# Optimization experiments

Hardware: AMD Instinct MI355X
Metric: run time of the kernel (lower is better)

Reference implementation:

```python
import jax, jax.numpy as jnp
import numpy as np

D_MODEL, D_INNER, D_STATE, D_CONV, DT_RANK = 1024, 2048, 16, 4, 64
BATCH, SEQLEN = 4, 2048


def setup_inputs() -> dict:
    key = jax.random.key(0)
    ks = jax.random.split(key, 10)
    def n(k, shape, scale=1.0):
        return (jax.random.normal(k, shape, dtype=jnp.float32) * scale)
    # A_log = log of positive values in (0, d_state] like the torch init
    A_log = jnp.log(jax.random.uniform(ks[7], (D_INNER, D_STATE), dtype=jnp.float32, minval=0.5, maxval=float(D_STATE)))
    return {
        "hidden_states": n(ks[0], (BATCH, SEQLEN, D_MODEL)),
        "in_proj_w": n(ks[1], (2 * D_INNER, D_MODEL), D_MODEL ** -0.5),
        "conv_w": n(ks[2], (D_INNER, D_CONV), D_CONV ** -0.5),
        "conv_b": n(ks[3], (D_INNER,), 0.1),
        "x_proj_w": n(ks[4], (DT_RANK + 2 * D_STATE, D_INNER), D_INNER ** -0.5),
        "dt_proj_w": n(ks[5], (D_INNER, DT_RANK), DT_RANK ** -0.5),
        "dt_proj_b": n(ks[6], (D_INNER,), 0.5),
        "A_log": A_log,
        "D": jnp.ones((D_INNER,), dtype=jnp.float32),
        "out_proj_w": n(ks[8], (D_MODEL, D_INNER), D_INNER ** -0.5),
    }


def _silu(x):
    return x * jax.nn.sigmoid(x)


def _mamba_forward(hidden_states, in_proj_w, conv_w, conv_b, x_proj_w,
                   dt_proj_w, dt_proj_b, A_log, D, out_proj_w):
    B, L, _ = hidden_states.shape
    d_inner, d_conv = conv_w.shape
    d_state = A_log.shape[1]
    dt_rank = dt_proj_w.shape[1]

    # in_proj (no bias): (b, l, 2*d_inner)
    xz = jnp.einsum('bld,ed->ble', hidden_states, in_proj_w)
    x, z = xz[..., :d_inner], xz[..., d_inner:]

    # causal depthwise conv1d (padding = d_conv-1, truncated to L) + SiLU
    x_pad = jnp.pad(x, ((0, 0), (d_conv - 1, 0), (0, 0)))  # (b, L+d_conv-1, d)
    x_conv = sum(x_pad[:, w:w + L, :] * conv_w[:, w] for w in range(d_conv)) + conv_b
    x_conv = _silu(x_conv)  # (b, l, d_inner)

    # x_proj -> dt, B, C
    x_dbl = jnp.einsum('bld,ed->ble', x_conv, x_proj_w)  # (b, l, dt_rank+2*d_state)
    dt_in = x_dbl[..., :dt_rank]
    Bv = x_dbl[..., dt_rank:dt_rank + d_state]  # (b, l, n)
    Cv = x_dbl[..., dt_rank + d_state:]         # (b, l, n)

    delta = jax.nn.softplus(jnp.einsum('blr,dr->bld', dt_in, dt_proj_w) + dt_proj_b)
    A = -jnp.exp(A_log)  # (d, n), entries negative

    # selective scan over time: state h is (b, d, n)
    def step(h, inp):
        d_t, B_t, C_t, u_t = inp  # (b,d), (b,n), (b,n), (b,d)
        dA = jnp.exp(d_t[:, :, None] * A)                          # (b, d, n)
        h = h * dA + (d_t * u_t)[:, :, None] * B_t[:, None, :]     # (b, d, n)
        y = jnp.einsum('bdn,bn->bd', h, C_t)                       # (b, d)
        return h, y

    h0 = jnp.zeros((B, d_inner, d_state), dtype=hidden_states.dtype)
    xs = (jnp.swapaxes(delta, 0, 1), jnp.swapaxes(Bv, 0, 1),
          jnp.swapaxes(Cv, 0, 1), jnp.swapaxes(x_conv, 0, 1))
    _, ys = jax.lax.scan(step, h0, xs)  # (l, b, d)
    y = jnp.swapaxes(ys, 0, 1) + x_conv * D  # skip term D * u
    y = y * _silu(z)                           # gating

    # out_proj (no bias)
    return jnp.einsum('bld,md->blm', y, out_proj_w)


def reference(hidden_states, in_proj_w, conv_w, conv_b, x_proj_w,
              dt_proj_w, dt_proj_b, A_log, D, out_proj_w):
    return _mamba_forward(hidden_states, in_proj_w, conv_w, conv_b, x_proj_w,
                          dt_proj_w, dt_proj_b, A_log, D, out_proj_w)
```

## Files before the change

kernel.cpp:

```cpp
#include <hip/hip_runtime.h>
#include <hip/hip_bf16.h>

constexpr int BATCH = 4, SEQLEN = 2048, DM = 1024, DI = 2048, DS = 16, DC = 4, DTR = 64;
constexpr int M = BATCH * SEQLEN;
constexpr int NXZ = 2 * DI;
constexpr int NXDBL = DTR + 2 * DS;
constexpr int CL = 64;
constexpr int NCH = SEQLEN / CL;
constexpr size_t CS = (size_t)BATCH * DI * DS;
constexpr float L2E = 1.44269504088896f;

typedef __attribute__((ext_vector_type(8))) short short8;
typedef __attribute__((ext_vector_type(4))) float f32x4;
typedef __attribute__((ext_vector_type(2))) float f32x2;

__device__ __forceinline__ float fexp2(float x) { return __builtin_amdgcn_exp2f(x); }
__device__ __forceinline__ float frcp(float x) { return __builtin_amdgcn_rcpf(x); }
__device__ __forceinline__ float fsig(float z) {
  return frcp(1.f + fexp2(-L2E * z));
}
__device__ __forceinline__ float softplus_fast(float x) {
  return (x > 20.f) ? x
                    : 0.693147180559945f * __builtin_amdgcn_logf(1.f + fexp2(x * L2E));
}

__device__ __forceinline__ void load_lds16(const void* g, void* l) {
  __builtin_amdgcn_global_load_lds(
      (const __attribute__((address_space(1))) unsigned int*)g,
      (__attribute__((address_space(3))) unsigned int*)l, 16, 0, 0);
}

__global__ __launch_bounds__(256) void k_cvt(const float* __restrict__ s,
                                             __hip_bfloat16* __restrict__ d, int n) {
  int i = (blockIdx.x * 256 + threadIdx.x) * 8;
  if (i + 7 < n) {
    float4 v0 = *reinterpret_cast<const float4*>(s + i);
    float4 v1 = *reinterpret_cast<const float4*>(s + i + 4);
    unsigned short o[8];
    o[0] = __bfloat16_as_ushort(__float2bfloat16(v0.x));
    o[1] = __bfloat16_as_ushort(__float2bfloat16(v0.y));
    o[2] = __bfloat16_as_ushort(__float2bfloat16(v0.z));
    o[3] = __bfloat16_as_ushort(__float2bfloat16(v0.w));
    o[4] = __bfloat16_as_ushort(__float2bfloat16(v1.x));
    o[5] = __bfloat16_as_ushort(__float2bfloat16(v1.y));
    o[6] = __bfloat16_as_ushort(__float2bfloat16(v1.z));
    o[7] = __bfloat16_as_ushort(__float2bfloat16(v1.w));
    *reinterpret_cast<short8*>(d + i) = *reinterpret_cast<short8*>(o);
  }
}

__global__ __launch_bounds__(256) void k_cvt4(const float* __restrict__ p0, int n0, __hip_bfloat16* __restrict__ q0,
                                              const float* __restrict__ p1, int n1, __hip_bfloat16* __restrict__ q1,
                                              const float* __restrict__ p2, int n2, __hip_bfloat16* __restrict__ q2,
                                              const float* __restrict__ p3, int n3, __hip_bfloat16* __restrict__ q3) {
  int i = (blockIdx.x * 256 + threadIdx.x) * 8;
  const float* s;
  __hip_bfloat16* d;
  if (i < n0) { s = p0; d = q0; }
  else if ((i -= n0) < n1) { s = p1; d = q1; }
  else if ((i -= n1) < n2) { s = p2; d = q2; }
  else if ((i -= n2) < n3) { s = p3; d = q3; }
  else return;
  float4 v0 = *reinterpret_cast<const float4*>(s + i);
  float4 v1 = *reinterpret_cast<const float4*>(s + i + 4);
  unsigned short o[8];
  o[0] = __bfloat16_as_ushort(__float2bfloat16(v0.x));
  o[1] = __bfloat16_as_ushort(__float2bfloat16(v0.y));
  o[2] = __bfloat16_as_ushort(__float2bfloat16(v0.z));
  o[3] = __bfloat16_as_ushort(__float2bfloat16(v0.w));
  o[4] = __bfloat16_as_ushort(__float2bfloat16(v1.x));
  o[5] = __bfloat16_as_ushort(__float2bfloat16(v1.y));
  o[6] = __bfloat16_as_ushort(__float2bfloat16(v1.z));
  o[7] = __bfloat16_as_ushort(__float2bfloat16(v1.w));
  *reinterpret_cast<short8*>(d + i) = *reinterpret_cast<short8*>(o);
}

__global__ __launch_bounds__(256) void k_prep(const float* __restrict__ alog,
                                              float* __restrict__ an,
                                              const float* __restrict__ cw,
                                              float* __restrict__ cwt) {
  int i = blockIdx.x * 256 + threadIdx.x;
  if (i < DI * DS) {
    an[i] = -__expf(alog[i]) * L2E;
  } else {
    int j = i - DI * DS;
    if (j < DI * DC) {
      int d = j >> 2, w = j & 3;
      cwt[w * DI + d] = cw[j];
    }
  }
}

template <int BN, int OUTMODE, bool SWZ>
__global__ __launch_bounds__(512, 2) void k_gemmp(const __hip_bfloat16* __restrict__ A, int lda,
                                                  const __hip_bfloat16* __restrict__ Bm, int ldb,
                                                  void* __restrict__ Cp, int ldc, int K) {
  constexpr int BK = 64;
  constexpr int ASLOT = 16384;
  constexpr int BSLOT = BN * BK;
  constexpr int FN = (BN / 4) / 16;
  constexpr int BBASE = 2 * ASLOT;

  const int tid = threadIdx.x;
  const int wid = tid >> 6, l = tid & 63;
  const int wr = wid >> 2, wc = wid & 3;

  int bx = blockIdx.x, by = blockIdx.y;
  if constexpr (SWZ) {
    const int gx = gridDim.x;
    int nlin = by * gx + bx;
    const int nwg = gx * gridDim.y;
    nlin = (nlin & 7) * (nwg >> 3) + (nlin >> 3);
    by = nlin / gx; bx = nlin % gx;
  }
  const int bm0 = by * 256, bn0 = bx * BN;
  const int NT = K / BK;

  __shared__ short LDS[2 * (ASLOT + BSLOT)];

  const int gc8 = (l & 7) ^ ((l >> 3) & 7);
  const __hip_bfloat16* Abase = A + (size_t)(bm0 + wid * 8 + (l >> 3)) * lda + gc8 * 8;
  const __hip_bfloat16* Bbase = Bm + (size_t)(bn0 + wid * 8 + (l >> 3)) * ldb + gc8 * 8;
  const int wslot = wid * 512;

  const int c8k0 = ((l >> 4) ^ (l & 7)) * 8;
  const int c8k1 = ((4 + (l >> 4)) ^ (l & 7)) * 8;
  const int aoff0 = wr * 8192 + (l & 15) * 64;
  const int boff0 = BBASE + wc * (BN / 4) * 64 + (l & 15) * 64;

  f32x4 acc[8][FN] = {};

  auto stageA = [&](int s, int kt) {
#pragma unroll
    for (int g = 0; g < 4; g++)
      load_lds16(Abase + (size_t)(g * 64) * lda + kt * BK,
                 &LDS[s * ASLOT + g * 4096 + wslot]);
  };
  auto stageB = [&](int s, int kt) {
#pragma unroll
    for (int g = 0; g < BN / 64; g++)
      load_lds16(Bbase + (size_t)(g * 64) * ldb + kt * BK,
                 &LDS[BBASE + s * BSLOT + g * 4096 + wslot]);
  };

  stageA(0, 0); stageB(0, 0);

  for (int t = 0; t < NT; t++) {
    const int d = t & 1;
    asm volatile("s_waitcnt vmcnt(0)" ::: "memory");
    __builtin_amdgcn_s_barrier();
    if (t + 1 < NT) { stageA(d ^ 1, t + 1); stageB(d ^ 1, t + 1); }

    const int adb = d * ASLOT + aoff0;
    const int bdb = d * BSLOT + boff0;
    short8 a0[4][2], a1[4][2], b[FN][2];
#pragma unroll
    for (int i = 0; i < 4; i++) {
      a0[i][0] = *reinterpret_cast<const short8*>(&LDS[adb + i * 1024 + c8k0]);
      a0[i][1] = *reinterpret_cast<const short8*>(&LDS[adb + i * 1024 + c8k1]);
    }
#pragma unroll
    for (int j = 0; j < FN; j++) {
      b[j][0] = *reinterpret_cast<const short8*>(&LDS[bdb + j * 1024 + c8k0]);
      b[j][1] = *reinterpret_cast<const short8*>(&LDS[bdb + j * 1024 + c8k1]);
    }
#pragma unroll
    for (int i = 0; i < 4; i++) {
      a1[i][0] = *reinterpret_cast<const short8*>(&LDS[adb + (4 + i) * 1024 + c8k0]);
      a1[i][1] = *reinterpret_cast<const short8*>(&LDS[adb + (4 + i) * 1024 + c8k1]);
    }
#pragma unroll
    for (int i = 0; i < 4; i++)
#pragma unroll
      for (int j = 0; j < FN; j++)
#pragma unroll
        for (int ks = 0; ks < 2; ks++) {
          acc[i][j] = __builtin_amdgcn_mfma_f32_16x16x32_bf16(a0[i][ks], b[j][ks], acc[i][j], 0, 0, 0);
          acc[4 + i][j] = __builtin_amdgcn_mfma_f32_16x16x32_bf16(a1[i][ks], b[j][ks], acc[4 + i][j], 0, 0, 0);
        }
  }

  const int crow0 = bm0 + wr * 128 + (l >> 4) * 4;
  const int ccol0 = bn0 + wc * (BN / 4) + (l & 15);
#pragma unroll
  for (int im = 0; im < 8; im++)
#pragma unroll
    for (int jn = 0; jn < FN; jn++) {
      const int col = ccol0 + jn * 16;
#pragma unroll
      for (int r = 0; r < 4; r++) {
        const int row = crow0 + im * 16 + r;
        float v = acc[im][jn][r];
        if constexpr (OUTMODE == 0)
          reinterpret_cast<float*>(Cp)[(size_t)row * ldc + col] = v;
        else
          reinterpret_cast<__hip_bfloat16*>(Cp)[(size_t)row * ldc + col] = __float2bfloat16(v);
      }
    }
}

template <int BM, int BN, int OUTMODE>
__global__ __launch_bounds__(256) void k_gemm_dl(const __hip_bfloat16* __restrict__ A, int lda,
                                                 const __hip_bfloat16* __restrict__ Bm, int ldb,
                                                 void* __restrict__ Cp, int ldc, int K,
                                                 const float* __restrict__ bias) {
  constexpr int BK = 32;
  constexpr int WM = BM / 2, WN = BN / 2;
  constexpr int FM = WM / 16, FN = WN / 16;

  const int tid = threadIdx.x;
  const int wid = tid >> 6, lane = tid & 63;
  const int wm = wid >> 1, wn = wid & 1;
  const int bm0 = blockIdx.y * BM, bn0 = blockIdx.x * BN;
  int kz = 0;
  if constexpr (OUTMODE == 4) kz = blockIdx.z;

  __shared__ short As[BM * BK];
  __shared__ short Bs[BN * BK];

  f32x4 acc[FM][FN] = {};

  const int lrow = lane & 15;
  const int lk = (lane >> 4) * 8;
  const int srow = wid * 16 + (lane >> 2);
  const int scol = (lane & 3) * 8;

  const __hip_bfloat16* Ag = &A[(size_t)(bm0 + srow) * lda + scol + (size_t)kz * K];
  const __hip_bfloat16* Bg = &Bm[(size_t)(bn0 + srow) * ldb + scol + (size_t)kz * K];

  for (int k0 = 0; k0 < K; k0 += BK) {
    __syncthreads();
#pragma unroll
    for (int i = 0; i < (BM + 63) / 64; i++)
      load_lds16(Ag + (size_t)i * 64 * lda + k0, &As[(i * 64 + wid * 16) * BK]);
#pragma unroll
    for (int i = 0; i < (BN + 63) / 64; i++)
      if ((BN % 64 == 0) || (i * 64 + wid * 16 < BN))
        load_lds16(Bg + (size_t)i * 64 * ldb + k0, &Bs[(i * 64 + wid * 16) * BK]);
    __syncthreads();

    short8 af[FM], bf[FN];
#pragma unroll
    for (int i = 0; i < FM; i++)
      af[i] = *reinterpret_cast<const short8*>(&As[(wm * WM + i * 16 + lrow) * BK + lk]);
#pragma unroll
    for (int j = 0; j < FN; j++)
      bf[j] = *reinterpret_cast<const short8*>(&Bs[(wn * WN + j * 16 + lrow) * BK + lk]);
#pragma unroll
    for (int i = 0; i < FM; i++)
#pragma unroll
      for (int j = 0; j < FN; j++)
        acc[i][j] = __builtin_amdgcn_mfma_f32_16x16x32_bf16(af[i], bf[j], acc[i][j], 0, 0, 0);
  }

  const int crow0 = bm0 + wm * WM + (lane >> 4) * 4;
  const int ccol0 = bn0 + wn * WN + lrow;
#pragma unroll
  for (int i = 0; i < FM; i++)
#pragma unroll
    for (int j = 0; j < FN; j++) {
      const int col = ccol0 + j * 16;
      float bv = 0.f;
      if constexpr (OUTMODE == 2) bv = bias[col];
#pragma unroll
      for (int r = 0; r < 4; r++) {
        const int row = crow0 + i * 16 + r;
        float v = acc[i][j][r];
        if constexpr (OUTMODE == 0) {
          reinterpret_cast<float*>(Cp)[(size_t)row * ldc + col] = v;
        } else if constexpr (OUTMODE == 2) {
          reinterpret_cast<__hip_bfloat16*>(Cp)[(size_t)row * ldc + col] =
              __float2bfloat16(softplus_fast(v + bv));
        } else {
          reinterpret_cast<float*>(Cp)[(size_t)kz * M * NXDBL + (size_t)row * ldc + col] = v;
        }
      }
    }
}

__global__ __launch_bounds__(256) void k_xred(const float* __restrict__ part,
                                              float* __restrict__ xdbl,
                                              __hip_bfloat16* __restrict__ dtin) {
  int i = (blockIdx.x * 256 + threadIdx.x) * 4;
  float4 s = *reinterpret_cast<const float4*>(part + i);
#pragma unroll
  for (int p = 1; p < 8; p++) {
    const float4 v = *reinterpret_cast<const float4*>(part + (size_t)p * M * NXDBL + i);
    s.x += v.x; s.y += v.y; s.z += v.z; s.w += v.w;
  }
  *reinterpret_cast<float4*>(xdbl + i) = s;
  int c = i % NXDBL;
  if (c < DTR) {
    int m = i / NXDBL;
    __hip_bfloat16* dp = dtin + (size_t)m * DTR + c;
    dp[0] = __float2bfloat16(s.x);
    dp[1] = __float2bfloat16(s.y);
    dp[2] = __float2bfloat16(s.z);
    dp[3] = __float2bfloat16(s.w);
  }
}

__global__ __launch_bounds__(256) void k_conv8(const __hip_bfloat16* __restrict__ xz,
                                               const float* __restrict__ cwt,
                                               const float* __restrict__ cb,
                                               __hip_bfloat16* __restrict__ xc) {
  const int ml = blockIdx.x;
  const int d0 = threadIdx.x * 8;
  const int l = ml & (SEQLEN - 1);
  float acc[8];
  {
    float4 b0 = *reinterpret_cast<const float4*>(cb + d0);
    float4 b1 = *reinterpret_cast<const float4*>(cb + d0 + 4);
    acc[0] = b0.x; acc[1] = b0.y; acc[2] = b0.z; acc[3] = b0.w;
    acc[4] = b1.x; acc[5] = b1.y; acc[6] = b1.z; acc[7] = b1.w;
  }
#pragma unroll
  for (int w = 0; w < DC; w++) {
    int li = l - 3 + w;
    if (li >= 0) {
      short8 xv = *reinterpret_cast<const short8*>(&xz[(size_t)(ml - 3 + w) * NXZ + d0]);
      float4 w0 = *reinterpret_cast<const float4*>(cwt + w * DI + d0);
      float4 w1 = *reinterpret_cast<const float4*>(cwt + w * DI + d0 + 4);
      float wf[8] = {w0.x, w0.y, w0.z, w0.w, w1.x, w1.y, w1.z, w1.w};
#pragma unroll
      for (int j = 0; j < 8; j++) {
        float x = __bfloat162float(__ushort_as_bfloat16((unsigned short)xv[j]));
        acc[j] = fmaf(x, wf[j], acc[j]);
      }
    }
  }
  unsigned short o[8];
#pragma unroll
  for (int j = 0; j < 8; j++)
    o[j] = __bfloat16_as_ushort(__float2bfloat16(acc[j] * fsig(acc[j])));
  *reinterpret_cast<short8*>(&xc[(size_t)ml * DI + d0]) = *reinterpret_cast<short8*>(o);
}

__global__ __launch_bounds__(256) void k_scan1(const __hip_bfloat16* __restrict__ delta_b,
                                               const float* __restrict__ xdbl,
                                               const __hip_bfloat16* __restrict__ xc,
                                               const float* __restrict__ Aneg2,
                                               __hip_bfloat16* __restrict__ Pb,
                                               __hip_bfloat16* __restrict__ Sb) {
  const int tid = threadIdx.x;
  const int d = blockIdx.x * 256 + tid;
  const int c = blockIdx.y, b = blockIdx.z;
  const size_t row0 = (size_t)b * SEQLEN + (size_t)c * CL;

  __shared__ float Bs[CL][16];
  {
    int i = tid * 4;
    int li = i >> 4, n0 = i & 15;
    const float* src = &xdbl[(row0 + li) * NXDBL + DTR + n0];
    *reinterpret_cast<float4*>(&Bs[li][n0]) = *reinterpret_cast<const float4*>(src);
  }

  f32x2 Ar2[8];
#pragma unroll
  for (int p = 0; p < 8; p++)
    Ar2[p] = *reinterpret_cast<const f32x2*>(&Aneg2[d * DS + 2 * p]);
  __syncthreads();

  f32x2 h2[8] = {};
  float sdelta = 0.f;
  size_t idx = row0 * DI + d;
  float nx_dt = __bfloat162float(delta_b[idx]);
  float nx_u = __bfloat162float(xc[idx]);
  for (int ls = 0; ls < CL; ls++) {
    float delta = nx_dt;
    float u = nx_u;
    if (ls + 1 < CL) {
      size_t idx2 = idx + DI;
      nx_dt = __bfloat162float(delta_b[idx2]);
      nx_u = __bfloat162float(xc[idx2]);
    }
    idx += DI;
    sdelta += delta;
    float du = delta * u;
    f32x2 delta2 = {delta, delta};
    f32x2 du2 = {du, du};
#pragma unroll
    for (int p = 0; p < 8; p++) {
      f32x2 arg = delta2 * Ar2[p];
      f32x2 dA = {fexp2(arg.x), fexp2(arg.y)};
      f32x2 t = du2 * *reinterpret_cast<const f32x2*>(&Bs[ls][2 * p]);
      h2[p] = __builtin_elementwise_fma(h2[p], dA, t);
    }
  }

  size_t base = (size_t)c * CS + ((size_t)b * DI + d) * DS;
  unsigned short sp[DS], ss[DS];
#pragma unroll
  for (int p = 0; p < 8; p++) {
    ss[2 * p] = __bfloat16_as_ushort(__float2bfloat16(h2[p].x));
    ss[2 * p + 1] = __bfloat16_as_ushort(__float2bfloat16(h2[p].y));
    sp[2 * p] = __bfloat16_as_ushort(__float2bfloat16(fexp2(Ar2[p].x * sdelta)));
    sp[2 * p + 1] = __bfloat16_as_ushort(__float2bfloat16(fexp2(Ar2[p].y * sdelta)));
  }
#pragma unroll
  for (int q = 0; q < 2; q++) {
    *reinterpret_cast<short8*>(&Sb[base + q * 8]) = *reinterpret_cast<short8*>(&ss[q * 8]);
    *reinterpret_cast<short8*>(&Pb[base + q * 8]) = *reinterpret_cast<short8*>(&sp[q * 8]);
  }
}

__global__ __launch_bounds__(256) void k_scan2(const __hip_bfloat16* __restrict__ Pb,
                                               const __hip_bfloat16* __restrict__ Sb,
                                               __hip_bfloat16* __restrict__ Hin) {
  size_t t = (size_t)blockIdx.x * 256 + threadIdx.x;
  float h = 0.f;
  for (int c = 0; c < NCH; c++) {
    size_t o = (size_t)c * CS + t;
    Hin[o] = __float2bfloat16(h);
    h = fmaf(__bfloat162float(Pb[o]), h, __bfloat162float(Sb[o]));
  }
}

__global__ __launch_bounds__(256) void k_scan3(const __hip_bfloat16* __restrict__ delta_b,
                                               const float* __restrict__ xdbl,
                                               const __hip_bfloat16* __restrict__ xc,
                                               const __hip_bfloat16* __restrict__ xz,
                                               const float* __restrict__ Aneg2,
                                               const float* __restrict__ Dw,
                                               const __hip_bfloat16* __restrict__ Hin,
                                               __hip_bfloat16* __restrict__ yg) {
  const int tid = threadIdx.x;
  const int d = blockIdx.x * 256 + tid;
  const int c = blockIdx.y, b = blockIdx.z;
  const size_t row0 = (size_t)b * SEQLEN + (size_t)c * CL;

  __shared__ float BCs[CL][32];
  {
    int i = tid * 8;
    int li = i >> 5, n0 = i & 31;
    const float* src = &xdbl[(row0 + li) * NXDBL + DTR + n0];
    *reinterpret_cast<float4*>(&BCs[li][n0]) = *reinterpret_cast<const float4*>(src);
    *reinterpret_cast<float4*>(&BCs[li][n0 + 4]) = *reinterpret_cast<const float4*>(src + 4);
  }

  f32x2 Ar2[8];
#pragma unroll
  for (int p = 0; p < 8; p++)
    Ar2[p] = *reinterpret_cast<const f32x2*>(&Aneg2[d * DS + 2 * p]);
  const float Dv = Dw[d];

  f32x2 h2[8];
  {
    size_t hbase = (size_t)c * CS + ((size_t)b * DI + d) * DS;
#pragma unroll
    for (int q = 0; q < 2; q++) {
      short8 hv = *reinterpret_cast<const short8*>(&Hin[hbase + q * 8]);
#pragma unroll
      for (int p = 0; p < 4; p++) {
        h2[q * 4 + p].x = __bfloat162float(__ushort_as_bfloat16((unsigned short)hv[2 * p]));
        h2[q * 4 + p].y = __bfloat162float(__ushort_as_bfloat16((unsigned short)hv[2 * p + 1]));
      }
    }
  }
  __syncthreads();

  size_t idx = row0 * DI + d;
  float nx_dt = __bfloat162float(delta_b[idx]);
  float nx_u = __bfloat162float(xc[idx]);
  float nx_z = __bfloat162float(xz[row0 * NXZ + DI + d]);
  for (int ls = 0; ls < CL; ls++) {
    const size_t cur = idx;
    float delta = nx_dt;
    float u = nx_u;
    float zv = nx_z;
    if (ls + 1 < CL) {
      size_t idx2 = idx + DI;
      nx_dt = __bfloat162float(delta_b[idx2]);
      nx_u = __bfloat162float(xc[idx2]);
      nx_z = __bfloat162float(xz[(row0 + ls + 1) * NXZ + DI + d]);
    }
    idx += DI;
    float du = delta * u;
    f32x2 delta2 = {delta, delta};
    f32x2 du2 = {du, du};
    f32x2 y20 = {0.f, 0.f}, y21 = {0.f, 0.f}, y22 = {0.f, 0.f}, y23 = {0.f, 0.f};
#pragma unroll
    for (int p = 0; p < 8; p++) {
      f32x2 arg = delta2 * Ar2[p];
      f32x2 dA = {fexp2(arg.x), fexp2(arg.y)};
      f32x2 t = du2 * *reinterpret_cast<const f32x2*>(&BCs[ls][2 * p]);
      h2[p] = __builtin_elementwise_fma(h2[p], dA, t);
      const f32x2 cv = *reinterpret_cast<const f32x2*>(&BCs[ls][16 + 2 * p]);
      if (p == 0 || p == 4) y20 = __builtin_elementwise_fma(h2[p], cv, y20);
      else if (p == 1 || p == 5) y21 = __builtin_elementwise_fma(h2[p], cv, y21);
      else if (p == 2 || p == 6) y22 = __builtin_elementwise_fma(h2[p], cv, y22);
      else y23 = __builtin_elementwise_fma(h2[p], cv, y23);
    }
    f32x2 ys = (y20 + y21) + (y22 + y23);
    float y = ys.x + ys.y;
    float out = (y + u * Dv) * (zv * fsig(zv));
    yg[cur] = __float2bfloat16(out);
  }
}

extern "C" void kernel_launch(void* const* d_in, const int* in_sizes, int n_in,
                              void* d_out, int out_size, void* d_ws, size_t ws_size,
                              hipStream_t stream) {
  const float* hs = (const float*)d_in[0];
  const float* w_in = (const float*)d_in[1];
  const float* conv_w = (const float*)d_in[2];
  const float* conv_b = (const float*)d_in[3];
  const float* w_xp = (const float*)d_in[4];
  const float* w_dt = (const float*)d_in[5];
  const float* dt_b = (const float*)d_in[6];
  const float* A_log = (const float*)d_in[7];
  const float* Dw = (const float*)d_in[8];
  const float* w_out = (const float*)d_in[9];
  float* out = (float*)d_out;

  char* ws = (char*)d_ws;
  size_t off = 0;
  auto alloc = [&](size_t bytes) {
    void* p = ws + off;
    off += (bytes + 255) & ~(size_t)255;
    return p;
  };

  __hip_bfloat16* hs_b   = (__hip_bfloat16*)alloc((size_t)M * DM * 2);
  __hip_bfloat16* win_b  = (__hip_bfloat16*)alloc((size_t)NXZ * DM * 2);
  __hip_bfloat16* wxp_b  = (__hip_bfloat16*)alloc((size_t)NXDBL * DI * 2);
  __hip_bfloat16* wdt_b  = (__hip_bfloat16*)alloc((size_t)DI * DTR * 2);
  __hip_bfloat16* wout_b = (__hip_bfloat16*)alloc((size_t)DM * DI * 2);
  float*          Aneg2  = (float*)alloc((size_t)DI * DS * 4);
  float*          cwt    = (float*)alloc((size_t)DC * DI * 4);
  __hip_bfloat16* xz_b   = (__hip_bfloat16*)alloc((size_t)M * NXZ * 2);
  __hip_bfloat16* xc_b   = (__hip_bfloat16*)alloc((size_t)M * DI * 2);
  float*          xdbl   = (float*)alloc((size_t)M * NXDBL * 4);
  __hip_bfloat16* dtin_b = (__hip_bfloat16*)alloc((size_t)M * DTR * 2);
  __hip_bfloat16* delta_b= (__hip_bfloat16*)alloc((size_t)M * DI * 2);
  __hip_bfloat16* yg_b   = (__hip_bfloat16*)alloc((size_t)M * DI * 2);

  float* xpart = (float*)(ws + 0);
  __hip_bfloat16* Pb  = (__hip_bfloat16*)(ws + 0);
  __hip_bfloat16* Sb  = (__hip_bfloat16*)(ws + ((size_t)8 << 20));
  __hip_bfloat16* Hin = (__hip_bfloat16*)(ws + ((size_t)16 << 20));

  k_cvt<<<(M * DM) / 2048, 256, 0, stream>>>(hs, hs_b, M * DM);
  k_cvt4<<<(NXZ * DM + NXDBL * DI + DI * DTR + DM * DI) / 2048, 256, 0, stream>>>(
      w_in, NXZ * DM, win_b, w_xp, NXDBL * DI, wxp_b, w_dt, DI * DTR, wdt_b,
      w_out, DM * DI, wout_b);
  k_prep<<<(DI * DS + DI * DC + 255) / 256, 256, 0, stream>>>(A_log, Aneg2, conv_w, cwt);

  k_gemmp<256, 1, false><<<dim3(NXZ / 256, M / 256), 512, 0, stream>>>(
      hs_b, DM, win_b, DM, xz_b, NXZ, DM);

  k_conv8<<<M, 256, 0, stream>>>(xz_b, cwt, conv_b, xc_b);

  k_gemm_dl<64, 96, 4><<<dim3(1, M / 64, 8), 256, 0, stream>>>(
      xc_b, DI, wxp_b, DI, xpart, NXDBL, DI / 8, nullptr);
  k_xred<<<(M * NXDBL) / 1024, 256, 0, stream>>>(xpart, xdbl, dtin_b);

  k_gemm_dl<64, 128, 2><<<dim3(DI / 128, M / 64), 256, 0, stream>>>(
      dtin_b, DTR, wdt_b, DTR, delta_b, DI, DTR, dt_b);

  k_scan1<<<dim3(DI / 256, NCH, BATCH), 256, 0, stream>>>(delta_b, xdbl, xc_b,
                                                          Aneg2, Pb, Sb);
  k_scan2<<<(int)(CS / 256), 256, 0, stream>>>(Pb, Sb, Hin);
  k_scan3<<<dim3(DI / 256, NCH, BATCH), 256, 0, stream>>>(delta_b, xdbl, xc_b,
                                                          xz_b, Aneg2, Dw, Hin, yg_b);

  k_gemmp<128, 0, true><<<dim3(DM / 128, M / 256), 512, 0, stream>>>(
      yg_b, DI, wout_b, DI, out, DM, DI);
}
```

Baseline: 288.6 us.

## Rework bf16 GEMM with BK=32 tiles, new LDS swizzle and MFMA priority boost

Rewrites the double-buffered bf16 GEMM used for in_proj and out_proj. The K tile shrinks from 64 to 32, which halves LDS use per block, and the staging and fragment-read layout gets a new XOR swizzle for the 32-wide rows. s_setprio is raised around the MFMA loop. The aim is higher occupancy and less bank conflict, at the cost of twice as many barriers and K iterations, each with less compute to hide load latency.

```diff
diff --git a/kernel.cpp b/kernel.cpp
--- a/kernel.cpp
+++ b/kernel.cpp
@@ -92,14 +92,14 @@
 }
 
 template <int BN, int OUTMODE, bool SWZ>
-__global__ __launch_bounds__(512, 2) void k_gemmp(const __hip_bfloat16* __restrict__ A, int lda,
+__global__ __launch_bounds__(512, 2) void k_gemm2(const __hip_bfloat16* __restrict__ A, int lda,
                                                   const __hip_bfloat16* __restrict__ Bm, int ldb,
                                                   void* __restrict__ Cp, int ldc, int K) {
-  constexpr int BK = 64;
-  constexpr int ASLOT = 16384;
-  constexpr int BSLOT = BN * BK;
-  constexpr int FN = (BN / 4) / 16;
-  constexpr int BBASE = 2 * ASLOT;
+  constexpr int BK = 32;
+  constexpr int ASL = 256 * BK;
+  constexpr int BSL = BN * BK;
+  constexpr int SLOT = ASL + BSL;
+  constexpr int FN = BN / 64;
 
   const int tid = threadIdx.x;
   const int wid = tid >> 6, l = tid & 63;
@@ -116,68 +116,57 @@
   const int bm0 = by * 256, bn0 = bx * BN;
   const int NT = K / BK;
 
-  __shared__ short LDS[2 * (ASLOT + BSLOT)];
-
-  const int gc8 = (l & 7) ^ ((l >> 3) & 7);
-  const __hip_bfloat16* Abase = A + (size_t)(bm0 + wid * 8 + (l >> 3)) * lda + gc8 * 8;
-  const __hip_bfloat16* Bbase = Bm + (size_t)(bn0 + wid * 8 + (l >> 3)) * ldb + gc8 * 8;
-  const int wslot = wid * 512;
-
-  const int c8k0 = ((l >> 4) ^ (l & 7)) * 8;
-  const int c8k1 = ((4 + (l >> 4)) ^ (l & 7)) * 8;
-  const int aoff0 = wr * 8192 + (l & 15) * 64;
-  const int boff0 = BBASE + wc * (BN / 4) * 64 + (l & 15) * 64;
+  __shared__ short LDS[2 * SLOT];
+
+  const int srow = tid >> 2;
+  const int sc8 = ((tid & 3) ^ ((srow >> 1) & 3)) * 8;
+  const __hip_bfloat16* Abase = A + (size_t)(bm0 + srow) * lda + sc8;
+  const __hip_bfloat16* Bbase = Bm + (size_t)(bn0 + srow) * ldb + sc8;
+  const int wdst = wid * 512;
+
+  const int cp8 = ((l >> 4) ^ (((l & 15) >> 1) & 3)) * 8;
+  const int abase_l = (wr * 128 + (l & 15)) * BK + cp8;
+  const int bbase_l = ASL + (wc * (BN / 4) + (l & 15)) * BK + cp8;
 
   f32x4 acc[8][FN] = {};
 
   auto stageA = [&](int s, int kt) {
 #pragma unroll
-    for (int g = 0; g < 4; g++)
-      load_lds16(Abase + (size_t)(g * 64) * lda + kt * BK,
-                 &LDS[s * ASLOT + g * 4096 + wslot]);
+    for (int g = 0; g < 2; g++)
+      load_lds16(Abase + (size_t)(g * 128) * lda + kt * BK,
+                 &LDS[s * SLOT + g * 4096 + wdst]);
   };
   auto stageB = [&](int s, int kt) {
 #pragma unroll
-    for (int g = 0; g < BN / 64; g++)
-      load_lds16(Bbase + (size_t)(g * 64) * ldb + kt * BK,
-                 &LDS[BBASE + s * BSLOT + g * 4096 + wslot]);
+    for (int g = 0; g < BN / 128; g++)
+      load_lds16(Bbase + (size_t)(g * 128) * ldb + kt * BK,
+                 &LDS[s * SLOT + ASL + g * 4096 + wdst]);
   };
 
   stageA(0, 0); stageB(0, 0);
 
   for (int t = 0; t < NT; t++) {
-    const int d = t & 1;
+    const int s = t & 1;
     asm volatile("s_waitcnt vmcnt(0)" ::: "memory");
     __builtin_amdgcn_s_barrier();
-    if (t + 1 < NT) { stageA(d ^ 1, t + 1); stageB(d ^ 1, t + 1); }
-
-    const int adb = d * ASLOT + aoff0;
-    const int bdb = d * BSLOT + boff0;
-    short8 a0[4][2], a1[4][2], b[FN][2];
-#pragma unroll
-    for (int i = 0; i < 4; i++) {
-      a0[i][0] = *reinterpret_cast<const short8*>(&LDS[adb + i * 1024 + c8k0]);
-      a0[i][1] = *reinterpret_cast<const short8*>(&LDS[adb + i * 1024 + c8k1]);
-    }
-#pragma unroll
-    for (int j = 0; j < FN; j++) {
-      b[j][0] = *reinterpret_cast<const short8*>(&LDS[bdb + j * 1024 + c8k0]);
-      b[j][1] = *reinterpret_cast<const short8*>(&LDS[bdb + j * 1024 + c8k1]);
-    }
-#pragma unroll
-    for (int i = 0; i < 4; i++) {
-      a1[i][0] = *reinterpret_cast<const short8*>(&LDS[adb + (4 + i) * 1024 + c8k0]);
-      a1[i][1] = *reinterpret_cast<const short8*>(&LDS[adb + (4 + i) * 1024 + c8k1]);
-    }
-#pragma unroll
-    for (int i = 0; i < 4; i++)
+    if (t + 1 < NT) { stageA(s ^ 1, t + 1); stageB(s ^ 1, t + 1); }
+
+    const int ab = s * SLOT + abase_l;
+    const int bb = s * SLOT + bbase_l;
+    short8 a[8], b[FN];
+#pragma unroll
+    for (int i = 0; i < 8; i++)
+      a[i] = *reinterpret_cast<const short8*>(&LDS[ab + i * 512]);
+#pragma unroll
+    for (int j = 0; j < FN; j++)
+      b[j] = *reinterpret_cast<const short8*>(&LDS[bb + j * 512]);
+    __builtin_amdgcn_s_setprio(1);
+#pragma unroll
+    for (int i = 0; i < 8; i++)
 #pragma unroll
       for (int j = 0; j < FN; j++)
-#pragma unroll
-        for (int ks = 0; ks < 2; ks++) {
-          acc[i][j] = __builtin_amdgcn_mfma_f32_16x16x32_bf16(a0[i][ks], b[j][ks], acc[i][j], 0, 0, 0);
-          acc[4 + i][j] = __builtin_amdgcn_mfma_f32_16x16x32_bf16(a1[i][ks], b[j][ks], acc[4 + i][j], 0, 0, 0);
-        }
+        acc[i][j] = __builtin_amdgcn_mfma_f32_16x16x32_bf16(a[i], b[j], acc[i][j], 0, 0, 0);
+    __builtin_amdgcn_s_setprio(0);
   }
 
   const int crow0 = bm0 + wr * 128 + (l >> 4) * 4;
@@ -546,7 +535,7 @@
       w_out, DM * DI, wout_b);
   k_prep<<<(DI * DS + DI * DC + 255) / 256, 256, 0, stream>>>(A_log, Aneg2, conv_w, cwt);
 
-  k_gemmp<256, 1, false><<<dim3(NXZ / 256, M / 256), 512, 0, stream>>>(
+  k_gemm2<256, 1, false><<<dim3(NXZ / 256, M / 256), 512, 0, stream>>>(
       hs_b, DM, win_b, DM, xz_b, NXZ, DM);
 
   k_conv8<<<M, 256, 0, stream>>>(xz_b, cwt, conv_b, xc_b);
@@ -564,6 +553,6 @@
   k_scan3<<<dim3(DI / 256, NCH, BATCH), 256, 0, stream>>>(delta_b, xdbl, xc_b,
                                                           xz_b, Aneg2, Dw, Hin, yg_b);
 
-  k_gemmp<128, 0, true><<<dim3(DM / 128, M / 256), 512, 0, stream>>>(
+  k_gemm2<128, 0, true><<<dim3(DM / 128, M / 256), 512, 0, stream>>>(
       yg_b, DI, wout_b, DI, out, DM, DI);
 }
```

Measured after the change: 302.2 us. 4.7% more time.
